# Kernel tuning notes

Measured on AMD Instinct MI355X. Metric: run time of the kernel, lower is better.

## Reference

```python
import jax, jax.numpy as jnp
import numpy as np

B, S, D, H = 4, 1024, 1024, 16
HD = D // H
EPS = 1e-5


def setup_inputs() -> dict:
    key = jax.random.key(0)
    ks = jax.random.split(key, 12)
    sc = 0.02
    return {
        "x": jax.random.normal(ks[0], (B, S, D), jnp.float32),
        "WQ": jax.random.normal(ks[1], (D, D), jnp.float32) * sc,
        "WK": jax.random.normal(ks[2], (D, D), jnp.float32) * sc,
        "WV": jax.random.normal(ks[3], (D, D), jnp.float32) * sc,
        "Wo": jax.random.normal(ks[4], (D, D), jnp.float32) * sc,
        "bo": jnp.zeros((D,), jnp.float32),
        "W1": jax.random.normal(ks[5], (D, 4 * D), jnp.float32) * sc,
        "b1": jnp.zeros((4 * D,), jnp.float32),
        "W2": jax.random.normal(ks[6], (4 * D, D), jnp.float32) * sc,
        "b2": jnp.zeros((D,), jnp.float32),
        "ln1_s": jnp.ones((D,), jnp.float32),
        "ln1_b": jnp.zeros((D,), jnp.float32),
        "ln2_s": jnp.ones((D,), jnp.float32),
        "ln2_b": jnp.zeros((D,), jnp.float32),
    }


def _layernorm(x, scale, shift):
    mean = jnp.mean(x, axis=-1, keepdims=True)
    var = jnp.mean((x - mean) ** 2, axis=-1, keepdims=True)  # unbiased=False
    return scale * ((x - mean) / jnp.sqrt(var + EPS)) + shift


def _gelu(x):
    c = jnp.sqrt(2.0 / jnp.pi).astype(x.dtype)
    return 0.5 * x * (1.0 + jnp.tanh(c * (x + 0.044715 * x ** 3)))


def reference(x, WQ, WK, WV, Wo, bo, W1, b1, W2, b2, ln1_s, ln1_b, ln2_s, ln2_b):
    b, s, d = x.shape
    # --- attention sub-block (pre-norm) ---
    h = _layernorm(x, ln1_s, ln1_b)
    q = (h @ WQ).reshape(b, s, H, HD).transpose(0, 2, 1, 3)  # [B,H,S,HD]
    k = (h @ WK).reshape(b, s, H, HD).transpose(0, 2, 1, 3)
    v = (h @ WV).reshape(b, s, H, HD).transpose(0, 2, 1, 3)
    scores = jnp.einsum("bhqd,bhkd->bhqk", q, k)
    causal = jnp.triu(jnp.ones((s, s), dtype=bool), k=1)
    scores = jnp.where(causal, -jnp.inf, scores)
    attn = jax.nn.softmax(scores / jnp.sqrt(jnp.float32(HD)), axis=-1)
    ctx = jnp.einsum("bhqk,bhkd->bhqd", attn, v)
    ctx = ctx.transpose(0, 2, 1, 3).reshape(b, s, d)
    x = x + (ctx @ Wo + bo)
    # --- FF sub-block (pre-norm) ---
    h = _layernorm(x, ln2_s, ln2_b)
    h = _gelu(h @ W1 + b1)
    return x + (h @ W2 + b2)
```

## Files before the change

kernel.cpp:

```cpp
#include <hip/hip_runtime.h>
#include <hip/hip_bf16.h>

#define DIM   1024
#define NHEAD 16
#define HDIM  64
#define BATCH 4
#define SEQ   1024
#define MTOT  (BATCH*SEQ)
#define DFF   (4*DIM)
#define LDQ   3072

typedef _Float16 f16x8 __attribute__((ext_vector_type(8)));
typedef _Float16 f16x4 __attribute__((ext_vector_type(4)));
typedef float    f32x4 __attribute__((ext_vector_type(4)));

__device__ __forceinline__ float geluf(float x) {
    float z2 = 1.5957691216057308f * (x + 0.044715f * x * x * x);
    return x * __builtin_amdgcn_rcpf(1.0f + __expf(-z2));
}

__device__ __forceinline__ int swz_off(int row, int slot) {
    return row * 128 + ((slot ^ (row & 7)) << 4);
}
__device__ __forceinline__ f16x8 ldsfrag(const _Float16* s, int row, int slot) {
    return *(const f16x8*)((const char*)s + swz_off(row, slot));
}

template <int NCHUNK>
__device__ __forceinline__ void stage_async(const _Float16* __restrict__ g, int ld,
                                            _Float16* s, int w, int lane) {
    int r_in = lane >> 3;
    int sslot = lane & 7;
    int lslot = sslot ^ r_in;
#pragma unroll
    for (int q = 0; q < NCHUNK; ++q) {
        int chunk = w * NCHUNK + q;
        int row = chunk * 8 + r_in;
        const _Float16* gp = g + (size_t)row * ld + lslot * 8;
        _Float16* sp = s + chunk * 512;
        __builtin_amdgcn_global_load_lds(
            (const __attribute__((address_space(1))) void*)gp,
            (__attribute__((address_space(3))) void*)sp, 16, 0, 0);
    }
}

__global__ __launch_bounds__(256) void k_tcvt(const float* __restrict__ src,
                                              _Float16* __restrict__ dst,
                                              int K, int N) {
    __shared__ float tile[32][33];
    int n0 = blockIdx.x * 32, k0 = blockIdx.y * 32;
    int tx = threadIdx.x, ty = threadIdx.y;
#pragma unroll
    for (int i = 0; i < 32; i += 8)
        tile[ty + i][tx] = src[(size_t)(k0 + ty + i) * N + (n0 + tx)];
    __syncthreads();
#pragma unroll
    for (int i = 0; i < 32; i += 8)
        dst[(size_t)(n0 + ty + i) * K + (k0 + tx)] = (_Float16)tile[tx][ty + i];
}

__global__ __launch_bounds__(256) void k_tcvt3(const float* __restrict__ s0,
                                               const float* __restrict__ s1,
                                               const float* __restrict__ s2,
                                               _Float16* __restrict__ dst) {
    __shared__ float tile[32][33];
    const float* src = blockIdx.z == 0 ? s0 : (blockIdx.z == 1 ? s1 : s2);
    _Float16* d = dst + (size_t)blockIdx.z * (1024 * 1024);
    int n0 = blockIdx.x * 32, k0 = blockIdx.y * 32;
    int tx = threadIdx.x, ty = threadIdx.y;
#pragma unroll
    for (int i = 0; i < 32; i += 8)
        tile[ty + i][tx] = src[(size_t)(k0 + ty + i) * 1024 + (n0 + tx)];
    __syncthreads();
#pragma unroll
    for (int i = 0; i < 32; i += 8)
        d[(size_t)(n0 + ty + i) * 1024 + (k0 + tx)] = (_Float16)tile[tx][ty + i];
}

__global__ __launch_bounds__(256) void k_ln(const float* __restrict__ x,
                                            const float* __restrict__ sc,
                                            const float* __restrict__ sh,
                                            _Float16* __restrict__ out) {
    int row = blockIdx.x;
    int t = threadIdx.x;
    float4 v = ((const float4*)(x + (size_t)row * DIM))[t];
    float sum = v.x + v.y + v.z + v.w;
    float sq  = v.x * v.x + v.y * v.y + v.z * v.z + v.w * v.w;
#pragma unroll
    for (int m = 1; m < 64; m <<= 1) {
        sum += __shfl_xor(sum, m);
        sq  += __shfl_xor(sq, m);
    }
    __shared__ float rs[4], rq[4];
    int w = t >> 6;
    if ((t & 63) == 0) { rs[w] = sum; rq[w] = sq; }
    __syncthreads();
    sum = rs[0] + rs[1] + rs[2] + rs[3];
    sq  = rq[0] + rq[1] + rq[2] + rq[3];
    float mean = sum * (1.0f / DIM);
    float var  = sq * (1.0f / DIM) - mean * mean;
    float rstd = rsqrtf(var + 1e-5f);
    float4 s4 = ((const float4*)sc)[t];
    float4 b4 = ((const float4*)sh)[t];
    f16x4 o;
    o[0] = (_Float16)(s4.x * ((v.x - mean) * rstd) + b4.x);
    o[1] = (_Float16)(s4.y * ((v.y - mean) * rstd) + b4.y);
    o[2] = (_Float16)(s4.z * ((v.z - mean) * rstd) + b4.z);
    o[3] = (_Float16)(s4.w * ((v.w - mean) * rstd) + b4.w);
    ((f16x4*)(out + (size_t)row * DIM))[t] = o;
}

template <int EPI>
__global__ __launch_bounds__(256) void k_gemm(const _Float16* __restrict__ A,
                                              const _Float16* __restrict__ BT,
                                              int M, int N, int K,
                                              _Float16* __restrict__ Ch,
                                              const float* __restrict__ bias) {
    __shared__ _Float16 As[2][128 * 64];
    __shared__ _Float16 Bs[2][128 * 64];
    int t = threadIdx.x;
    int m0 = blockIdx.y * 128, n0 = blockIdx.x * 128;
    int lane = t & 63, w = t >> 6;
    int wm = (w >> 1) * 64, wn = (w & 1) * 64;
    int lr = lane & 15, lg = lane >> 4;
    f32x4 acc[4][4];
#pragma unroll
    for (int i = 0; i < 4; ++i)
#pragma unroll
        for (int j = 0; j < 4; ++j) acc[i][j] = (f32x4){0.f, 0.f, 0.f, 0.f};

    const _Float16* Ag = A  + (size_t)m0 * K;
    const _Float16* Bg = BT + (size_t)n0 * K;
    int nt = K / 64;
    stage_async<4>(Ag, K, As[0], w, lane);
    stage_async<4>(Bg, K, Bs[0], w, lane);
    __syncthreads();
    for (int tt = 0; tt < nt; ++tt) {
        int cur = tt & 1, nxt = cur ^ 1;
        if (tt + 1 < nt) {
            stage_async<4>(Ag + (tt + 1) * 64, K, As[nxt], w, lane);
            stage_async<4>(Bg + (tt + 1) * 64, K, Bs[nxt], w, lane);
        }
#pragma unroll
        for (int kk = 0; kk < 2; ++kk) {
            f16x8 a[4], b[4];
#pragma unroll
            for (int i = 0; i < 4; ++i) a[i] = ldsfrag(As[cur], wm + i * 16 + lr, kk * 4 + lg);
#pragma unroll
            for (int j = 0; j < 4; ++j) b[j] = ldsfrag(Bs[cur], wn + j * 16 + lr, kk * 4 + lg);
            __builtin_amdgcn_s_setprio(1);
#pragma unroll
            for (int i = 0; i < 4; ++i)
#pragma unroll
                for (int j = 0; j < 4; ++j)
                    acc[i][j] = __builtin_amdgcn_mfma_f32_16x16x32_f16(a[i], b[j], acc[i][j], 0, 0, 0);
            __builtin_amdgcn_s_setprio(0);
        }
        __syncthreads();
    }
#pragma unroll
    for (int i = 0; i < 4; ++i) {
#pragma unroll
        for (int j = 0; j < 4; ++j) {
            int row = m0 + wm + i * 16 + lg * 4;
            int col = n0 + wn + j * 16 + lr;
#pragma unroll
            for (int r = 0; r < 4; ++r) {
                float v = acc[i][j][r];
                size_t idx = (size_t)(row + r) * N + col;
                if constexpr (EPI == 0) Ch[idx] = (_Float16)v;
                else                    Ch[idx] = (_Float16)geluf(v + bias[col]);
            }
        }
    }
}

__global__ __launch_bounds__(256) void k_gemm64(const _Float16* __restrict__ A,
                                                const _Float16* __restrict__ BT,
                                                int M, int N, int K,
                                                float* __restrict__ Cf,
                                                const float* __restrict__ bias,
                                                const float* __restrict__ resid) {
    __shared__ _Float16 As[2][128 * 64];
    __shared__ _Float16 Bs[2][64 * 64];
    int t = threadIdx.x;
    int m0 = blockIdx.y * 128, n0 = blockIdx.x * 64;
    int lane = t & 63, w = t >> 6;
    int wm = w * 32;
    int lr = lane & 15, lg = lane >> 4;
    f32x4 acc[2][4];
#pragma unroll
    for (int i = 0; i < 2; ++i)
#pragma unroll
        for (int j = 0; j < 4; ++j) acc[i][j] = (f32x4){0.f, 0.f, 0.f, 0.f};

    const _Float16* Ag = A  + (size_t)m0 * K;
    const _Float16* Bg = BT + (size_t)n0 * K;
    int nt = K / 64;
    stage_async<4>(Ag, K, As[0], w, lane);
    stage_async<2>(Bg, K, Bs[0], w, lane);
    __syncthreads();
    for (int tt = 0; tt < nt; ++tt) {
        int cur = tt & 1, nxt = cur ^ 1;
        if (tt + 1 < nt) {
            stage_async<4>(Ag + (tt + 1) * 64, K, As[nxt], w, lane);
            stage_async<2>(Bg + (tt + 1) * 64, K, Bs[nxt], w, lane);
        }
#pragma unroll
        for (int kk = 0; kk < 2; ++kk) {
            f16x8 a[2], b[4];
#pragma unroll
            for (int i = 0; i < 2; ++i) a[i] = ldsfrag(As[cur], wm + i * 16 + lr, kk * 4 + lg);
#pragma unroll
            for (int j = 0; j < 4; ++j) b[j] = ldsfrag(Bs[cur], j * 16 + lr, kk * 4 + lg);
            __builtin_amdgcn_s_setprio(1);
#pragma unroll
            for (int i = 0; i < 2; ++i)
#pragma unroll
                for (int j = 0; j < 4; ++j)
                    acc[i][j] = __builtin_amdgcn_mfma_f32_16x16x32_f16(a[i], b[j], acc[i][j], 0, 0, 0);
            __builtin_amdgcn_s_setprio(0);
        }
        __syncthreads();
    }
#pragma unroll
    for (int i = 0; i < 2; ++i) {
#pragma unroll
        for (int j = 0; j < 4; ++j) {
            int row = m0 + wm + i * 16 + lg * 4;
            int col = n0 + j * 16 + lr;
#pragma unroll
            for (int r = 0; r < 4; ++r) {
                size_t idx = (size_t)(row + r) * N + col;
                Cf[idx] = acc[i][j][r] + bias[col] + resid[idx];
            }
        }
    }
}

__global__ __launch_bounds__(64) void k_attn(const _Float16* __restrict__ QKV,
                                             _Float16* __restrict__ Og) {
    __shared__ _Float16 Vt[64 * 64];
    __shared__ _Float16 Ps[32 * 64];
    int lane = threadIdx.x;
    int id = blockIdx.x;
    int bh = id & 63;
    int qt = (SEQ / 32 - 1) - (id >> 6);
    int h = bh & 15, b = bh >> 4;
    int q0 = qt * 32;
    int lr = lane & 15, lg = lane >> 4;
    size_t base = (size_t)b * SEQ;
    int cq = h * HDIM, ck = 1024 + h * HDIM, cv = 2048 + h * HDIM;

    f16x8 aq[2][2];
#pragma unroll
    for (int i = 0; i < 2; ++i)
#pragma unroll
        for (int kk = 0; kk < 2; ++kk) {
            f16x8 v = *(const f16x8*)(QKV + (base + q0 + i * 16 + lr) * LDQ + cq + kk * 32 + lg * 8);
#pragma unroll
            for (int e = 0; e < 8; ++e) v[e] = v[e] * (_Float16)0.125f;
            aq[i][kk] = v;
        }

    f32x4 cacc[2][4];
#pragma unroll
    for (int i = 0; i < 2; ++i)
#pragma unroll
        for (int j = 0; j < 4; ++j) cacc[i][j] = (f32x4){0.f, 0.f, 0.f, 0.f};
    float mrun[2][4], lrun[2][4];
#pragma unroll
    for (int i = 0; i < 2; ++i)
#pragma unroll
        for (int r = 0; r < 4; ++r) { mrun[i][r] = -1e30f; lrun[i][r] = 0.f; }

    int ntiles = q0 / 64 + 1;
    for (int kt = 0; kt < ntiles; ++kt) {
        int k0 = kt * 64;
        {
            const _Float16* vr = QKV + (base + k0 + lane) * LDQ + cv;
            int kslot = lane >> 3;
            int kb2 = (lane & 7) * 2;
#pragma unroll
            for (int part = 0; part < 8; ++part) {
                f16x8 v8 = *(const f16x8*)(vr + part * 8);
#pragma unroll
                for (int e = 0; e < 8; ++e) {
                    int d = part * 8 + e;
                    *(_Float16*)((char*)Vt + d * 128 + ((kslot ^ (d & 7)) << 4) + kb2) = v8[e];
                }
            }
        }
        f32x4 sacc[2][4];
#pragma unroll
        for (int i = 0; i < 2; ++i)
#pragma unroll
            for (int j = 0; j < 4; ++j) sacc[i][j] = (f32x4){0.f, 0.f, 0.f, 0.f};
#pragma unroll
        for (int kk = 0; kk < 2; ++kk) {
            f16x8 bk[4];
#pragma unroll
            for (int j = 0; j < 4; ++j)
                bk[j] = *(const f16x8*)(QKV + (base + k0 + j * 16 + lr) * LDQ + ck + kk * 32 + lg * 8);
            __builtin_amdgcn_s_setprio(1);
#pragma unroll
            for (int i = 0; i < 2; ++i)
#pragma unroll
                for (int j = 0; j < 4; ++j)
                    sacc[i][j] = __builtin_amdgcn_mfma_f32_16x16x32_f16(aq[i][kk], bk[j], sacc[i][j], 0, 0, 0);
            __builtin_amdgcn_s_setprio(0);
        }
        if (kt == ntiles - 1) {
#pragma unroll
            for (int i = 0; i < 2; ++i)
#pragma unroll
                for (int j = 0; j < 4; ++j)
#pragma unroll
                    for (int r = 0; r < 4; ++r) {
                        int qq = q0 + i * 16 + lg * 4 + r;
                        int kc = k0 + j * 16 + lr;
                        if (kc > qq) sacc[i][j][r] = -1e30f;
                    }
        }
#pragma unroll
        for (int i = 0; i < 2; ++i) {
            float mn[4], al[4];
#pragma unroll
            for (int r = 0; r < 4; ++r) {
                float tm = fmaxf(fmaxf(sacc[i][0][r], sacc[i][1][r]),
                                 fmaxf(sacc[i][2][r], sacc[i][3][r]));
#pragma unroll
                for (int msk = 1; msk < 16; msk <<= 1) tm = fmaxf(tm, __shfl_xor(tm, msk));
                float m2 = fmaxf(mrun[i][r], tm);
                al[r] = __expf(mrun[i][r] - m2);
                mrun[i][r] = m2;
                mn[r] = m2;
            }
#pragma unroll
            for (int jd = 0; jd < 4; ++jd)
#pragma unroll
                for (int r = 0; r < 4; ++r) cacc[i][jd][r] *= al[r];
#pragma unroll
            for (int r = 0; r < 4; ++r) {
                float ps = 0.f;
#pragma unroll
                for (int j = 0; j < 4; ++j) {
                    float p = __expf(sacc[i][j][r] - mn[r]);
                    sacc[i][j][r] = p;
                    ps += p;
                }
#pragma unroll
                for (int msk = 1; msk < 16; msk <<= 1) ps += __shfl_xor(ps, msk);
                lrun[i][r] = lrun[i][r] * al[r] + ps;
            }
        }
#pragma unroll
        for (int i = 0; i < 2; ++i)
#pragma unroll
            for (int j = 0; j < 4; ++j) {
                int kc = j * 16 + lr;
                int ks = kc >> 3;
                int kb = (kc & 7) * 2;
#pragma unroll
                for (int r = 0; r < 4; ++r) {
                    int qq = i * 16 + lg * 4 + r;
                    *(_Float16*)((char*)Ps + qq * 128 + ((ks ^ (qq & 7)) << 4) + kb) =
                        (_Float16)sacc[i][j][r];
                }
            }
#pragma unroll
        for (int kk = 0; kk < 2; ++kk) {
            f16x8 pa[2], bv[4];
#pragma unroll
            for (int i = 0; i < 2; ++i)   pa[i]  = ldsfrag(Ps, i * 16 + lr,  kk * 4 + lg);
#pragma unroll
            for (int jd = 0; jd < 4; ++jd) bv[jd] = ldsfrag(Vt, jd * 16 + lr, kk * 4 + lg);
            __builtin_amdgcn_s_setprio(1);
#pragma unroll
            for (int i = 0; i < 2; ++i)
#pragma unroll
                for (int jd = 0; jd < 4; ++jd)
                    cacc[i][jd] = __builtin_amdgcn_mfma_f32_16x16x32_f16(pa[i], bv[jd], cacc[i][jd], 0, 0, 0);
            __builtin_amdgcn_s_setprio(0);
        }
    }
#pragma unroll
    for (int i = 0; i < 2; ++i)
#pragma unroll
        for (int jd = 0; jd < 4; ++jd)
#pragma unroll
            for (int r = 0; r < 4; ++r) {
                int qq = q0 + i * 16 + lg * 4 + r;
                int d = h * HDIM + jd * 16 + lr;
                Og[(base + qq) * DIM + d] = (_Float16)(cacc[i][jd][r] / lrun[i][r]);
            }
}

extern "C" void kernel_launch(void* const* d_in, const int* in_sizes, int n_in,
                              void* d_out, int out_size, void* d_ws, size_t ws_size,
                              hipStream_t stream) {
    const float* x    = (const float*)d_in[0];
    const float* WQ   = (const float*)d_in[1];
    const float* WK   = (const float*)d_in[2];
    const float* WV   = (const float*)d_in[3];
    const float* Wo   = (const float*)d_in[4];
    const float* bo   = (const float*)d_in[5];
    const float* W1   = (const float*)d_in[6];
    const float* b1   = (const float*)d_in[7];
    const float* W2   = (const float*)d_in[8];
    const float* b2   = (const float*)d_in[9];
    const float* ln1s = (const float*)d_in[10];
    const float* ln1b = (const float*)d_in[11];
    const float* ln2s = (const float*)d_in[12];
    const float* ln2b = (const float*)d_in[13];
    float* out = (float*)d_out;
    char* ws = (char*)d_ws;
    const size_t MB = 1024 * 1024;
    _Float16* WTqkv = (_Float16*)(ws + 0 * MB);
    _Float16* WTo   = (_Float16*)(ws + 6 * MB);
    _Float16* WT1   = (_Float16*)(ws + 8 * MB);
    _Float16* WT2   = (_Float16*)(ws + 16 * MB);
    _Float16* h1    = (_Float16*)(ws + 24 * MB);
    _Float16* qkvb  = (_Float16*)(ws + 32 * MB);
    _Float16* ctx   = (_Float16*)(ws + 56 * MB);
    _Float16* h2    = (_Float16*)(ws + 64 * MB);
    _Float16* ff1   = (_Float16*)(ws + 72 * MB);
    float*    x2    = (float*)   (ws + 104 * MB);

    dim3 tb(32, 8);
    k_tcvt3<<<dim3(32, 32, 3), tb, 0, stream>>>(WQ, WK, WV, WTqkv);
    k_tcvt<<<dim3(32, 32), tb, 0, stream>>>(Wo, WTo, 1024, 1024);
    k_tcvt<<<dim3(128, 32), tb, 0, stream>>>(W1, WT1, 1024, 4096);
    k_tcvt<<<dim3(32, 128), tb, 0, stream>>>(W2, WT2, 4096, 1024);

    k_ln<<<MTOT, 256, 0, stream>>>(x, ln1s, ln1b, h1);

    k_gemm<0><<<dim3(24, 32), 256, 0, stream>>>(h1, WTqkv, MTOT, LDQ, DIM, qkvb, nullptr);

    k_attn<<<dim3(2048), 64, 0, stream>>>(qkvb, ctx);

    k_gemm64<<<dim3(16, 32), 256, 0, stream>>>(ctx, WTo, MTOT, DIM, DIM, x2, bo, x);

    k_ln<<<MTOT, 256, 0, stream>>>(x2, ln2s, ln2b, h2);

    k_gemm<1><<<dim3(32, 32), 256, 0, stream>>>(h2, WT1, MTOT, DFF, DIM, ff1, b1);

    k_gemm64<<<dim3(16, 32), 256, 0, stream>>>(ff1, WT2, MTOT, DIM, DFF, out, b2, x2);
}
```

Before: 245.5 us.

## Unify GEMMs on 128x128 tiles with XCD-aware block remapping

Removes the 128x64 output-projection/FF2 GEMM kernel and runs those GEMMs through the 128x128 kernel with a new residual-add epilogue variant. Switches all GEMM launches to a 1D grid whose block IDs are remapped so that consecutive tiles land on the same XCD (blockIdx mod 8 grouping), improving L2 reuse of A/B panels. The larger tile raises arithmetic intensity, but the Wo and W2 GEMMs now launch only 256 blocks, which risks underfilling the 256 CUs, especially for the K=4096 FF2 GEMM.

```diff
diff --git a/kernel.cpp b/kernel.cpp
--- a/kernel.cpp
+++ b/kernel.cpp
@@ -113,13 +113,17 @@
 template <int EPI>
 __global__ __launch_bounds__(256) void k_gemm(const _Float16* __restrict__ A,
                                               const _Float16* __restrict__ BT,
-                                              int M, int N, int K,
+                                              int N, int K, int gx,
                                               _Float16* __restrict__ Ch,
-                                              const float* __restrict__ bias) {
+                                              float* __restrict__ Cf,
+                                              const float* __restrict__ bias,
+                                              const float* __restrict__ resid) {
     __shared__ _Float16 As[2][128 * 64];
     __shared__ _Float16 Bs[2][128 * 64];
     int t = threadIdx.x;
-    int m0 = blockIdx.y * 128, n0 = blockIdx.x * 128;
+    int bid = blockIdx.x;
+    int lin = (bid & 7) * ((int)gridDim.x >> 3) + (bid >> 3);
+    int m0 = (lin / gx) * 128, n0 = (lin % gx) * 128;
     int lane = t & 63, w = t >> 6;
     int wm = (w >> 1) * 64, wn = (w & 1) * 64;
     int lr = lane & 15, lg = lane >> 4;
@@ -168,71 +172,9 @@
             for (int r = 0; r < 4; ++r) {
                 float v = acc[i][j][r];
                 size_t idx = (size_t)(row + r) * N + col;
-                if constexpr (EPI == 0) Ch[idx] = (_Float16)v;
-                else                    Ch[idx] = (_Float16)geluf(v + bias[col]);
-            }
-        }
-    }
-}
-
-__global__ __launch_bounds__(256) void k_gemm64(const _Float16* __restrict__ A,
-                                                const _Float16* __restrict__ BT,
-                                                int M, int N, int K,
-                                                float* __restrict__ Cf,
-                                                const float* __restrict__ bias,
-                                                const float* __restrict__ resid) {
-    __shared__ _Float16 As[2][128 * 64];
-    __shared__ _Float16 Bs[2][64 * 64];
-    int t = threadIdx.x;
-    int m0 = blockIdx.y * 128, n0 = blockIdx.x * 64;
-    int lane = t & 63, w = t >> 6;
-    int wm = w * 32;
-    int lr = lane & 15, lg = lane >> 4;
-    f32x4 acc[2][4];
-#pragma unroll
-    for (int i = 0; i < 2; ++i)
-#pragma unroll
-        for (int j = 0; j < 4; ++j) acc[i][j] = (f32x4){0.f, 0.f, 0.f, 0.f};
-
-    const _Float16* Ag = A  + (size_t)m0 * K;
-    const _Float16* Bg = BT + (size_t)n0 * K;
-    int nt = K / 64;
-    stage_async<4>(Ag, K, As[0], w, lane);
-    stage_async<2>(Bg, K, Bs[0], w, lane);
-    __syncthreads();
-    for (int tt = 0; tt < nt; ++tt) {
-        int cur = tt & 1, nxt = cur ^ 1;
-        if (tt + 1 < nt) {
-            stage_async<4>(Ag + (tt + 1) * 64, K, As[nxt], w, lane);
-            stage_async<2>(Bg + (tt + 1) * 64, K, Bs[nxt], w, lane);
-        }
-#pragma unroll
-        for (int kk = 0; kk < 2; ++kk) {
-            f16x8 a[2], b[4];
-#pragma unroll
-            for (int i = 0; i < 2; ++i) a[i] = ldsfrag(As[cur], wm + i * 16 + lr, kk * 4 + lg);
-#pragma unroll
-            for (int j = 0; j < 4; ++j) b[j] = ldsfrag(Bs[cur], j * 16 + lr, kk * 4 + lg);
-            __builtin_amdgcn_s_setprio(1);
-#pragma unroll
-            for (int i = 0; i < 2; ++i)
-#pragma unroll
-                for (int j = 0; j < 4; ++j)
-                    acc[i][j] = __builtin_amdgcn_mfma_f32_16x16x32_f16(a[i], b[j], acc[i][j], 0, 0, 0);
-            __builtin_amdgcn_s_setprio(0);
-        }
-        __syncthreads();
-    }
-#pragma unroll
-    for (int i = 0; i < 2; ++i) {
-#pragma unroll
-        for (int j = 0; j < 4; ++j) {
-            int row = m0 + wm + i * 16 + lg * 4;
-            int col = n0 + j * 16 + lr;
-#pragma unroll
-            for (int r = 0; r < 4; ++r) {
-                size_t idx = (size_t)(row + r) * N + col;
-                Cf[idx] = acc[i][j][r] + bias[col] + resid[idx];
+                if constexpr (EPI == 0)      Ch[idx] = (_Float16)v;
+                else if constexpr (EPI == 1) Ch[idx] = (_Float16)geluf(v + bias[col]);
+                else                         Cf[idx] = v + bias[col] + resid[idx];
             }
         }
     }
@@ -435,15 +377,15 @@
 
     k_ln<<<MTOT, 256, 0, stream>>>(x, ln1s, ln1b, h1);
 
-    k_gemm<0><<<dim3(24, 32), 256, 0, stream>>>(h1, WTqkv, MTOT, LDQ, DIM, qkvb, nullptr);
+    k_gemm<0><<<dim3(768), 256, 0, stream>>>(h1, WTqkv, LDQ, DIM, 24, qkvb, nullptr, nullptr, nullptr);
 
     k_attn<<<dim3(2048), 64, 0, stream>>>(qkvb, ctx);
 
-    k_gemm64<<<dim3(16, 32), 256, 0, stream>>>(ctx, WTo, MTOT, DIM, DIM, x2, bo, x);
+    k_gemm<2><<<dim3(256), 256, 0, stream>>>(ctx, WTo, DIM, DIM, 8, nullptr, x2, bo, x);
 
     k_ln<<<MTOT, 256, 0, stream>>>(x2, ln2s, ln2b, h2);
 
-    k_gemm<1><<<dim3(32, 32), 256, 0, stream>>>(h2, WT1, MTOT, DFF, DIM, ff1, b1);
-
-    k_gemm64<<<dim3(16, 32), 256, 0, stream>>>(ff1, WT2, MTOT, DIM, DFF, out, b2, x2);
-}
+    k_gemm<1><<<dim3(1024), 256, 0, stream>>>(h2, WT1, DFF, DIM, 32, ff1, nullptr, b1, nullptr);
+
+    k_gemm<2><<<dim3(256), 256, 0, stream>>>(ff1, WT2, DIM, DFF, 8, nullptr, out, b2, x2);
+}
```

Result: slower. 257.4 us (+4.9%).
